# Kernel tuning notes

Measured on AMD Instinct MI355X. Metric: run time of the kernel, lower is better.

Reference implementation:

```python
import jax, jax.numpy as jnp
import numpy as np

LENGTH, D, CHI, CLASSES = 784, 2, 128, 10
BATCH = 1024


def setup_inputs() -> dict:
    key = jax.random.key(0)
    k1, k2, k3 = jax.random.split(key, 3)
    # feature-mapped samples (batch, d, length), values in [0,1] like cossin map
    x = jax.random.uniform(k1, (BATCH, D, LENGTH), dtype=jnp.float32)
    # per-site residual weights; small init so the residual recurrence stays stable
    W = jax.random.normal(k2, (LENGTH, D, CHI, CHI), dtype=jnp.float32) * (0.01 / np.sqrt(CHI))
    # classifier matrix applied to the final hidden vector
    V = jax.random.normal(k3, (CHI, CLASSES), dtype=jnp.float32) / np.sqrt(CHI)
    return {"x": x, "W": W, "V": V}


def reference(x, W, V):
    # x: (B, d, L), W: (L, d, chi, chi), V: (chi, classes)
    B = x.shape[0]
    chi = W.shape[2]
    h0 = jnp.ones((B, chi), dtype=x.dtype)  # initial hidden bond vector

    xs = jnp.moveaxis(x, 2, 0)  # (L, B, d) so scan iterates over sites

    def site_step(h, inputs):
        xn, Wn = inputs  # xn: (B, d), Wn: (d, chi, chi)
        # residual MPS update: h <- h + sum_{s,a} x[n,s] W_n[s,a,b] h[a]
        h = h + jnp.einsum('ns,sab,na->nb', xn, Wn, h)
        return h, None

    h, _ = jax.lax.scan(site_step, h0, (xs, W))
    logits = h @ V  # (B, classes)
    return logits
```

## Files before the change

kernel.cpp:

```cpp
#include <hip/hip_runtime.h>

#define LL 784
#define CHI 128
#define CLS 10
#define BC 16
#define NBLK 64
#define HS 132

typedef __attribute__((ext_vector_type(8))) short short8;
typedef __attribute__((ext_vector_type(4))) float floatx4;

__device__ inline unsigned int f2bf(float v) {
    unsigned int u = __float_as_uint(v);
    u += 0x7fffu + ((u >> 16) & 1u);
    return u >> 16;
}

__device__ inline void lds_barrier() {
    asm volatile("s_waitcnt lgkmcnt(0)\n\ts_barrier" ::: "memory");
}

__global__ __launch_bounds__(256) void prep_kernel(const float* __restrict__ W,
                                                   uint4* __restrict__ ws4) {
    int T = blockIdx.x * 256 + threadIdx.x;
    int n   = T >> 12;
    int rem = T & 4095;
    int F = rem >> 6;
    int l = rem & 63;
    int nt = F >> 3;
    int s  = (F >> 2) & 1;
    int kt = F & 3;
    int a0 = kt * 32 + (l >> 4) * 8;
    int c  = nt * 16 + (l & 15);
    const float* Wp = W + ((size_t)(n * 2 + s) * CHI + a0) * CHI + c;
    uint4 pk;
    pk.x = f2bf(Wp[0 * CHI]) | (f2bf(Wp[1 * CHI]) << 16);
    pk.y = f2bf(Wp[2 * CHI]) | (f2bf(Wp[3 * CHI]) << 16);
    pk.z = f2bf(Wp[4 * CHI]) | (f2bf(Wp[5 * CHI]) << 16);
    pk.w = f2bf(Wp[6 * CHI]) | (f2bf(Wp[7 * CHI]) << 16);
    ws4[T] = pk;
}

__global__ __launch_bounds__(512) void mps_kernel(const float* __restrict__ x,
                                                  const unsigned short* __restrict__ ws,
                                                  const float* __restrict__ V,
                                                  float* __restrict__ out) {
    __shared__ float hsh[BC * HS];
    __shared__ unsigned short afr_sh[4 * 64 * 8];
    __shared__ float xs[2 * 8 * 32];

    const int t = threadIdx.x;
    const int w = t >> 6, l = t & 63;
    const int m = l & 15, q = l >> 4;
    const int rb = blockIdx.x * BC;

    for (int i = t; i < BC * HS; i += 512) hsh[i] = 1.0f;

    const float* xrowp = x + (size_t)(rb + m) * (2 * LL) + (size_t)(q & 1) * LL;
    float4 xra, xrb, xra2, xrb2;
    if (l < 32) {
        xra = *(const float4*)(xrowp + 0);
        xrb = *(const float4*)(xrowp + 4);
        float xv[8] = {xra.x, xra.y, xra.z, xra.w, xrb.x, xrb.y, xrb.z, xrb.w};
        #pragma unroll
        for (int k = 0; k < 8; k++) xs[k * 32 + (q & 1) * 16 + m] = xv[k];
        xra2 = *(const float4*)(xrowp + 8);
        xrb2 = *(const float4*)(xrowp + 12);
    }
    __syncthreads();

    floatx4 hacc = (floatx4){1.f, 1.f, 1.f, 1.f};

    const unsigned short* wsw = ws + (size_t)w * 4096 + (size_t)(l << 3);
    short8 bA[2][4], bB[2][4];
    #pragma unroll
    for (int s2 = 0; s2 < 2; s2++)
        #pragma unroll
        for (int kt = 0; kt < 4; kt++) {
            bA[s2][kt] = *(const short8*)(wsw + (size_t)0 * 32768 + (s2 * 4 + kt) * 512);
            bB[s2][kt] = *(const short8*)(wsw + (size_t)1 * 32768 + (s2 * 4 + kt) * 512);
        }

#define SITE_BODY(NN, BUF, CHUNKW) do {                                          \
    const int n_ = (NN);                                                         \
    lds_barrier();                            \
    if ((CHUNKW) && l < 32) {                                                    \
        int par_ = (n_ >> 3) & 1;                                                \
        float xv_[8] = {xra2.x, xra2.y, xra2.z, xra2.w,                          \
                        xrb2.x, xrb2.y, xrb2.z, xrb2.w};                         \
        _Pragma("unroll")                                                        \
        for (int k = 0; k < 8; k++)                                              \
            xs[par_ * 256 + k * 32 + (q & 1) * 16 + m] = xv_[k];                 \
        if (n_ + 8 < LL) {                                                       \
            xra2 = *(const float4*)(xrowp + n_ + 8);                             \
            xrb2 = *(const float4*)(xrowp + n_ + 12);                            \
        }                                                                        \
    }                                                                            \
    if (w < 4) {            \
        int hb_ = m * HS + w * 32 + q * 8;                                       \
        floatx4 h0_ = *(const floatx4*)&hsh[hb_];                                \
        floatx4 h1_ = *(const floatx4*)&hsh[hb_ + 4];                            \
        uint4 pk_;                                                               \
        pk_.x = f2bf(h0_[0]) | (f2bf(h0_[1]) << 16);                             \
        pk_.y = f2bf(h0_[2]) | (f2bf(h0_[3]) << 16);                             \
        pk_.z = f2bf(h1_[0]) | (f2bf(h1_[1]) << 16);                             \
        pk_.w = f2bf(h1_[2]) | (f2bf(h1_[3]) << 16);                             \
        ((uint4*)afr_sh)[w * 64 + l] = pk_;                                      \
    }                                                                            \
    lds_barrier();                                \
    short8 af_[4];                                                               \
    _Pragma("unroll")                                                            \
    for (int kt = 0; kt < 4; kt++) af_[kt] = ((const short8*)afr_sh)[kt * 64 + l];\
    int xb_ = ((n_ >> 3) & 1) * 256 + (n_ & 7) * 32 + q * 4;                     \
    floatx4 x0v_ = *(const floatx4*)&xs[xb_];                                    \
    floatx4 x1v_ = *(const floatx4*)&xs[xb_ + 16];                               \
    floatx4 P0_ = (floatx4){0.f, 0.f, 0.f, 0.f};                                 \
    floatx4 P1_ = (floatx4){0.f, 0.f, 0.f, 0.f};                                 \
    _Pragma("unroll")                                                            \
    for (int kt = 0; kt < 4; kt++) {                                             \
        P0_ = __builtin_amdgcn_mfma_f32_16x16x32_bf16(af_[kt], BUF[0][kt], P0_, 0, 0, 0); \
        P1_ = __builtin_amdgcn_mfma_f32_16x16x32_bf16(af_[kt], BUF[1][kt], P1_, 0, 0, 0); \
    }                                                                            \
    if (n_ + 2 < LL) {                     \
        _Pragma("unroll")                                                        \
        for (int s2 = 0; s2 < 2; s2++)                                           \
            _Pragma("unroll")                                                    \
            for (int kt = 0; kt < 4; kt++)                                       \
                BUF[s2][kt] = *(const short8*)(wsw + (size_t)(n_ + 2) * 32768 +  \
                                               (s2 * 4 + kt) * 512);             \
    }                                                                            \
    _Pragma("unroll")                                                            \
    for (int i = 0; i < 4; i++)                                                  \
        hacc[i] += x0v_[i] * P0_[i] + x1v_[i] * P1_[i];                          \
    _Pragma("unroll")                                                            \
    for (int i = 0; i < 4; i++)                                                  \
        hsh[(q * 4 + i) * HS + w * 16 + m] = hacc[i];                            \
} while (0)

    for (int n = 0; n < LL; n += 2) {
        SITE_BODY(n, bA, ((n & 7) == 0 && n > 0));
        SITE_BODY(n + 1, bB, false);
    }
#undef SITE_BODY

    __syncthreads();

    if (t < BC * CLS) {
        int r = t / CLS, cls = t % CLS;
        float sum = 0.f;
        for (int a = 0; a < CHI; a++) sum += hsh[r * HS + a] * V[a * CLS + cls];
        out[(size_t)(rb + r) * CLS + cls] = sum;
    }
}

extern "C" void kernel_launch(void* const* d_in, const int* in_sizes, int n_in,
                              void* d_out, int out_size, void* d_ws, size_t ws_size,
                              hipStream_t stream) {
    const float* x = (const float*)d_in[0];
    const float* W = (const float*)d_in[1];
    const float* V = (const float*)d_in[2];
    float* out = (float*)d_out;

    prep_kernel<<<LL * 16, 256, 0, stream>>>(W, (uint4*)d_ws);
    mps_kernel<<<NBLK, 512, 0, stream>>>(x, (const unsigned short*)d_ws, V, out);
}
```

Measured before the change: 764.5 us.

## Double-buffer bf16 hidden fragments and drop one barrier per site

Each wave now writes its updated hidden state straight into a double-buffered bf16 A-fragment buffer in LDS, pairing neighbouring columns with a DPP lane swap. This removes the fp32 hidden staging array and the separate pack step, so each site needs one barrier instead of two. The MFMA chains are split into two independent accumulators to shorten the dependency chain. The prep kernel now stages W through an LDS tile to coalesce its reads. The fragment layout mapping is intricate and could be wrong.

```diff
diff --git a/kernel.cpp b/kernel.cpp
--- a/kernel.cpp
+++ b/kernel.cpp
@@ -5,7 +5,6 @@
 #define CLS 10
 #define BC 16
 #define NBLK 64
-#define HS 132
 
 typedef __attribute__((ext_vector_type(8))) short short8;
 typedef __attribute__((ext_vector_type(4))) float floatx4;
@@ -20,135 +19,155 @@
     asm volatile("s_waitcnt lgkmcnt(0)\n\ts_barrier" ::: "memory");
 }
 
+__device__ inline float dpp_xor1(float v) {
+    int r = __builtin_amdgcn_update_dpp(0, __float_as_int(v), 0xB1, 0xF, 0xF, true);
+    return __int_as_float(r);
+}
+
 __global__ __launch_bounds__(256) void prep_kernel(const float* __restrict__ W,
                                                    uint4* __restrict__ ws4) {
-    int T = blockIdx.x * 256 + threadIdx.x;
-    int n   = T >> 12;
-    int rem = T & 4095;
-    int F = rem >> 6;
-    int l = rem & 63;
-    int nt = F >> 3;
-    int s  = (F >> 2) & 1;
-    int kt = F & 3;
-    int a0 = kt * 32 + (l >> 4) * 8;
-    int c  = nt * 16 + (l & 15);
-    const float* Wp = W + ((size_t)(n * 2 + s) * CHI + a0) * CHI + c;
-    uint4 pk;
-    pk.x = f2bf(Wp[0 * CHI]) | (f2bf(Wp[1 * CHI]) << 16);
-    pk.y = f2bf(Wp[2 * CHI]) | (f2bf(Wp[3 * CHI]) << 16);
-    pk.z = f2bf(Wp[4 * CHI]) | (f2bf(Wp[5 * CHI]) << 16);
-    pk.w = f2bf(Wp[6 * CHI]) | (f2bf(Wp[7 * CHI]) << 16);
-    ws4[T] = pk;
+    __shared__ float tile[32 * 132];
+    const int b = blockIdx.x;
+    const int n = b >> 3, s = (b >> 2) & 1, kt = b & 3;
+    const float* Wp = W + ((size_t)(n * 2 + s) * CHI + kt * 32) * CHI;
+    const int t = threadIdx.x;
+    #pragma unroll
+    for (int k = 0; k < 4; k++) {
+        int v = t + k * 256;
+        int a = v >> 5, c4 = v & 31;
+        float4 val = *(const float4*)(Wp + a * CHI + c4 * 4);
+        *(float4*)&tile[a * 132 + c4 * 4] = val;
+    }
+    __syncthreads();
+    const int l = t & 63, f0 = t >> 6;
+    const int m_ = l & 15, q_ = l >> 4;
+    #pragma unroll
+    for (int ff = 0; ff < 2; ff++) {
+        int nt = f0 + ff * 4;
+        const float* tp = &tile[(q_ * 8) * 132 + nt * 16 + m_];
+        uint4 pk;
+        pk.x = f2bf(tp[0 * 132]) | (f2bf(tp[1 * 132]) << 16);
+        pk.y = f2bf(tp[2 * 132]) | (f2bf(tp[3 * 132]) << 16);
+        pk.z = f2bf(tp[4 * 132]) | (f2bf(tp[5 * 132]) << 16);
+        pk.w = f2bf(tp[6 * 132]) | (f2bf(tp[7 * 132]) << 16);
+        ws4[(size_t)(((n * 8 + nt) * 2 + s) * 4 + kt) * 64 + l] = pk;
+    }
 }
 
 __global__ __launch_bounds__(512) void mps_kernel(const float* __restrict__ x,
                                                   const unsigned short* __restrict__ ws,
                                                   const float* __restrict__ V,
                                                   float* __restrict__ out) {
-    __shared__ float hsh[BC * HS];
-    __shared__ unsigned short afr_sh[4 * 64 * 8];
-    __shared__ float xs[2 * 8 * 32];
+    __shared__ short8 afbuf[2][256];
+    __shared__ float xs[2][8][32];
+    __shared__ float hfin[16 * 132];
 
     const int t = threadIdx.x;
     const int w = t >> 6, l = t & 63;
     const int m = l & 15, q = l >> 4;
     const int rb = blockIdx.x * BC;
 
-    for (int i = t; i < BC * HS; i += 512) hsh[i] = 1.0f;
+    for (int i = t; i < 1024; i += 512)
+        ((unsigned int*)&afbuf[0][0])[i] = 0x3F803F80u;
 
     const float* xrowp = x + (size_t)(rb + m) * (2 * LL) + (size_t)(q & 1) * LL;
-    float4 xra, xrb, xra2, xrb2;
+    float4 xc2a, xc2b;
     if (l < 32) {
-        xra = *(const float4*)(xrowp + 0);
-        xrb = *(const float4*)(xrowp + 4);
-        float xv[8] = {xra.x, xra.y, xra.z, xra.w, xrb.x, xrb.y, xrb.z, xrb.w};
+        float4 a0 = *(const float4*)(xrowp + 0);
+        float4 b0 = *(const float4*)(xrowp + 4);
+        float4 a1 = *(const float4*)(xrowp + 8);
+        float4 b1 = *(const float4*)(xrowp + 12);
+        float v0[8] = {a0.x, a0.y, a0.z, a0.w, b0.x, b0.y, b0.z, b0.w};
+        float v1[8] = {a1.x, a1.y, a1.z, a1.w, b1.x, b1.y, b1.z, b1.w};
         #pragma unroll
-        for (int k = 0; k < 8; k++) xs[k * 32 + (q & 1) * 16 + m] = xv[k];
-        xra2 = *(const float4*)(xrowp + 8);
-        xrb2 = *(const float4*)(xrowp + 12);
+        for (int k = 0; k < 8; k++) xs[0][k][(q & 1) * 16 + m] = v0[k];
+        #pragma unroll
+        for (int k = 0; k < 8; k++) xs[1][k][(q & 1) * 16 + m] = v1[k];
+        xc2a = *(const float4*)(xrowp + 16);
+        xc2b = *(const float4*)(xrowp + 20);
     }
+
+    const unsigned short* wsw = ws + (size_t)w * 4096 + (size_t)l * 8;
+    short8 bA[8], bB[8];
+    #pragma unroll
+    for (int f = 0; f < 8; f++) {
+        bA[f] = *(const short8*)(wsw + (size_t)0 * 32768 + f * 512);
+        bB[f] = *(const short8*)(wsw + (size_t)1 * 32768 + f * 512);
+    }
+
+    floatx4 hacc = (floatx4){1.f, 1.f, 1.f, 1.f};
+    const int kt_w = w >> 1;
+    const int qp_w = (w & 1) * 2 + (m >> 3);
+    const int col2 = (m & 7) >> 1;
+
     __syncthreads();
 
-    floatx4 hacc = (floatx4){1.f, 1.f, 1.f, 1.f};
-
-    const unsigned short* wsw = ws + (size_t)w * 4096 + (size_t)(l << 3);
-    short8 bA[2][4], bB[2][4];
-    #pragma unroll
-    for (int s2 = 0; s2 < 2; s2++)
-        #pragma unroll
-        for (int kt = 0; kt < 4; kt++) {
-            bA[s2][kt] = *(const short8*)(wsw + (size_t)0 * 32768 + (s2 * 4 + kt) * 512);
-            bB[s2][kt] = *(const short8*)(wsw + (size_t)1 * 32768 + (s2 * 4 + kt) * 512);
-        }
-
-#define SITE_BODY(NN, BUF, CHUNKW) do {                                          \
-    const int n_ = (NN);                                                         \
-    lds_barrier();                            \
-    if ((CHUNKW) && l < 32) {                                                    \
-        int par_ = (n_ >> 3) & 1;                                                \
-        float xv_[8] = {xra2.x, xra2.y, xra2.z, xra2.w,                          \
-                        xrb2.x, xrb2.y, xrb2.z, xrb2.w};                         \
-        _Pragma("unroll")                                                        \
-        for (int k = 0; k < 8; k++)                                              \
-            xs[par_ * 256 + k * 32 + (q & 1) * 16 + m] = xv_[k];                 \
-        if (n_ + 8 < LL) {                                                       \
-            xra2 = *(const float4*)(xrowp + n_ + 8);                             \
-            xrb2 = *(const float4*)(xrowp + n_ + 12);                            \
-        }                                                                        \
-    }                                                                            \
-    if (w < 4) {            \
-        int hb_ = m * HS + w * 32 + q * 8;                                       \
-        floatx4 h0_ = *(const floatx4*)&hsh[hb_];                                \
-        floatx4 h1_ = *(const floatx4*)&hsh[hb_ + 4];                            \
-        uint4 pk_;                                                               \
-        pk_.x = f2bf(h0_[0]) | (f2bf(h0_[1]) << 16);                             \
-        pk_.y = f2bf(h0_[2]) | (f2bf(h0_[3]) << 16);                             \
-        pk_.z = f2bf(h1_[0]) | (f2bf(h1_[1]) << 16);                             \
-        pk_.w = f2bf(h1_[2]) | (f2bf(h1_[3]) << 16);                             \
-        ((uint4*)afr_sh)[w * 64 + l] = pk_;                                      \
-    }                                                                            \
-    lds_barrier();                                \
-    short8 af_[4];                                                               \
-    _Pragma("unroll")                                                            \
-    for (int kt = 0; kt < 4; kt++) af_[kt] = ((const short8*)afr_sh)[kt * 64 + l];\
-    int xb_ = ((n_ >> 3) & 1) * 256 + (n_ & 7) * 32 + q * 4;                     \
-    floatx4 x0v_ = *(const floatx4*)&xs[xb_];                                    \
-    floatx4 x1v_ = *(const floatx4*)&xs[xb_ + 16];                               \
-    floatx4 P0_ = (floatx4){0.f, 0.f, 0.f, 0.f};                                 \
-    floatx4 P1_ = (floatx4){0.f, 0.f, 0.f, 0.f};                                 \
-    _Pragma("unroll")                                                            \
-    for (int kt = 0; kt < 4; kt++) {                                             \
-        P0_ = __builtin_amdgcn_mfma_f32_16x16x32_bf16(af_[kt], BUF[0][kt], P0_, 0, 0, 0); \
-        P1_ = __builtin_amdgcn_mfma_f32_16x16x32_bf16(af_[kt], BUF[1][kt], P1_, 0, 0, 0); \
-    }                                                                            \
-    if (n_ + 2 < LL) {                     \
-        _Pragma("unroll")                                                        \
-        for (int s2 = 0; s2 < 2; s2++)                                           \
-            _Pragma("unroll")                                                    \
-            for (int kt = 0; kt < 4; kt++)                                       \
-                BUF[s2][kt] = *(const short8*)(wsw + (size_t)(n_ + 2) * 32768 +  \
-                                               (s2 * 4 + kt) * 512);             \
-    }                                                                            \
-    _Pragma("unroll")                                                            \
-    for (int i = 0; i < 4; i++)                                                  \
-        hacc[i] += x0v_[i] * P0_[i] + x1v_[i] * P1_[i];                          \
-    _Pragma("unroll")                                                            \
-    for (int i = 0; i < 4; i++)                                                  \
-        hsh[(q * 4 + i) * HS + w * 16 + m] = hacc[i];                            \
+#define SITE_BODY(NN, BUF) do {                                                   \
+    const int n_ = (NN);                                                          \
+    lds_barrier();                                                                \
+    if ((n_ & 7) == 0 && n_ >= 8 && n_ + 8 < LL && l < 32) {                      \
+        int par_ = ((n_ >> 3) + 1) & 1;                                           \
+        float xv_[8] = {xc2a.x, xc2a.y, xc2a.z, xc2a.w,                           \
+                        xc2b.x, xc2b.y, xc2b.z, xc2b.w};                          \
+        _Pragma("unroll")                                                         \
+        for (int k = 0; k < 8; k++) xs[par_][k][(q & 1) * 16 + m] = xv_[k];       \
+        if (n_ + 16 < LL) {                                                       \
+            xc2a = *(const float4*)(xrowp + n_ + 16);                             \
+            xc2b = *(const float4*)(xrowp + n_ + 20);                             \
+        }                                                                         \
+    }                                                                             \
+    short8 af0 = afbuf[n_ & 1][0 * 64 + l];                                       \
+    short8 af1 = afbuf[n_ & 1][1 * 64 + l];                                       \
+    short8 af2 = afbuf[n_ & 1][2 * 64 + l];                                       \
+    short8 af3 = afbuf[n_ & 1][3 * 64 + l];                                       \
+    floatx4 x0v = *(const floatx4*)&xs[(n_ >> 3) & 1][n_ & 7][q * 4];             \
+    floatx4 x1v = *(const floatx4*)&xs[(n_ >> 3) & 1][n_ & 7][16 + q * 4];        \
+    floatx4 z = (floatx4){0.f, 0.f, 0.f, 0.f};                                    \
+    floatx4 a00 = __builtin_amdgcn_mfma_f32_16x16x32_bf16(af0, BUF[0], z, 0, 0, 0); \
+    floatx4 a01 = __builtin_amdgcn_mfma_f32_16x16x32_bf16(af2, BUF[2], z, 0, 0, 0); \
+    floatx4 a10 = __builtin_amdgcn_mfma_f32_16x16x32_bf16(af0, BUF[4], z, 0, 0, 0); \
+    floatx4 a11 = __builtin_amdgcn_mfma_f32_16x16x32_bf16(af2, BUF[6], z, 0, 0, 0); \
+    a00 = __builtin_amdgcn_mfma_f32_16x16x32_bf16(af1, BUF[1], a00, 0, 0, 0);     \
+    a01 = __builtin_amdgcn_mfma_f32_16x16x32_bf16(af3, BUF[3], a01, 0, 0, 0);     \
+    a10 = __builtin_amdgcn_mfma_f32_16x16x32_bf16(af1, BUF[5], a10, 0, 0, 0);     \
+    a11 = __builtin_amdgcn_mfma_f32_16x16x32_bf16(af3, BUF[7], a11, 0, 0, 0);     \
+    if (n_ + 2 < LL) {                                                            \
+        _Pragma("unroll")                                                         \
+        for (int f = 0; f < 8; f++)                                               \
+            BUF[f] = *(const short8*)(wsw + (size_t)(n_ + 2) * 32768 + f * 512);  \
+    }                                                                             \
+    _Pragma("unroll")                                                             \
+    for (int i = 0; i < 4; i++)                                                   \
+        hacc[i] += x0v[i] * (a00[i] + a01[i]) + x1v[i] * (a10[i] + a11[i]);       \
+    float pt0 = dpp_xor1(hacc[0]), pt1 = dpp_xor1(hacc[1]);                       \
+    float pt2 = dpp_xor1(hacc[2]), pt3 = dpp_xor1(hacc[3]);                       \
+    if (!(m & 1)) {                                                               \
+        unsigned int* dst = (unsigned int*)&afbuf[(n_ + 1) & 1][0];               \
+        int base_ = (kt_w * 64 + qp_w * 16 + q * 4) * 4 + col2;                   \
+        dst[base_ + 0 * 4] = f2bf(hacc[0]) | (f2bf(pt0) << 16);                   \
+        dst[base_ + 1 * 4] = f2bf(hacc[1]) | (f2bf(pt1) << 16);                   \
+        dst[base_ + 2 * 4] = f2bf(hacc[2]) | (f2bf(pt2) << 16);                   \
+        dst[base_ + 3 * 4] = f2bf(hacc[3]) | (f2bf(pt3) << 16);                   \
+    }                                                                             \
 } while (0)
 
     for (int n = 0; n < LL; n += 2) {
-        SITE_BODY(n, bA, ((n & 7) == 0 && n > 0));
-        SITE_BODY(n + 1, bB, false);
+        SITE_BODY(n, bA);
+        SITE_BODY(n + 1, bB);
     }
 #undef SITE_BODY
 
     __syncthreads();
 
+    #pragma unroll
+    for (int i = 0; i < 4; i++)
+        hfin[(q * 4 + i) * 132 + w * 16 + m] = hacc[i];
+    __syncthreads();
+
     if (t < BC * CLS) {
         int r = t / CLS, cls = t % CLS;
         float sum = 0.f;
-        for (int a = 0; a < CHI; a++) sum += hsh[r * HS + a] * V[a * CLS + cls];
+        for (int a = 0; a < CHI; a++) sum += hfin[r * 132 + a] * V[a * CLS + cls];
         out[(size_t)(rb + r) * CLS + cls] = sum;
     }
 }
@@ -161,6 +180,6 @@
     const float* V = (const float*)d_in[2];
     float* out = (float*)d_out;
 
-    prep_kernel<<<LL * 16, 256, 0, stream>>>(W, (uint4*)d_ws);
+    prep_kernel<<<LL * 8, 256, 0, stream>>>(W, (uint4*)d_ws);
     mps_kernel<<<NBLK, 512, 0, stream>>>(x, (const unsigned short*)d_ws, V, out);
 }
```

After: 683.0 us. 10.7% less time.
